# Performance work log

Hardware: AMD Instinct MI355X
Metric: run time of the kernel (lower is better)

Reference implementation:

```python
import jax, jax.numpy as jnp
import numpy as np

N = 1048576
B = 1024
H = 128
EPS = 1e-12  # F.normalize default eps


def setup_inputs() -> dict:
    key = jax.random.key(0)
    k1, k2, k3 = jax.random.split(key, 3)
    emb = jax.random.normal(k1, (N, H), dtype=jnp.float32)
    summary = jax.random.normal(k2, (B, H), dtype=jnp.float32)
    # CSR-style ptr: 0 = ptr[0] <= ... <= ptr[B] = N
    inner = jnp.sort(jax.random.randint(k3, (B - 1,), 0, N))
    ptr = jnp.concatenate([jnp.zeros((1,), jnp.int64),
                           inner.astype(jnp.int64),
                           jnp.full((1,), N, jnp.int64)])
    d = jnp.ones((H,), dtype=jnp.float32)
    scale = jnp.ones((1,), dtype=jnp.float32)
    return {"emb": emb, "summary": summary, "ptr": ptr, "d": d, "scale": scale}


def reference(emb, summary, ptr, d, scale):
    # L2-normalize each row (torch F.normalize: x / max(||x||, eps))
    norm = jnp.linalg.norm(emb, axis=-1, keepdims=True)
    emb_n = emb / jnp.maximum(norm, EPS)
    # node -> graph segment id from ptr (node i belongs to segment s iff ptr[s] <= i < ptr[s+1])
    seg = jnp.searchsorted(ptr[1:], jnp.arange(emb.shape[0]), side="right")  # [N]
    # fused diag-scale + per-graph ragged dot: out[n] = sum_h emb_n[n,h] * d[h] * summary[seg[n],h]
    s_per_node = summary[seg]  # [N, H] gather
    sim = jnp.sum(emb_n * d[None, :] * s_per_node, axis=-1)  # [N]
    return sim * scale[0]
```

## Files before the change

### kernel.cpp

```cpp
#include <hip/hip_runtime.h>
#include <math.h>


#define HDIM 128
#define NEPS 1e-12f

__global__ void seg_fill(const int* __restrict__ ptr, int* __restrict__ seg) {
    const int s  = blockIdx.x;
    const int lo = ptr[s], hi = ptr[s + 1];
    for (int i = lo + threadIdx.x; i < hi; i += blockDim.x)
        seg[i] = s;
}

__global__ void sd_fill(const float* __restrict__ summary,
                        const float* __restrict__ dvec,
                        const float* __restrict__ scale,
                        float* __restrict__ sd, int total) {
    const int i = blockIdx.x * blockDim.x + threadIdx.x;
    if (i < total) sd[i] = summary[i] * dvec[i & (HDIM - 1)] * scale[0];
}

__global__ __launch_bounds__(256) void sim_main(
    const float* __restrict__ emb,
    const float* __restrict__ sd,
    const int* __restrict__ seg,
    float* __restrict__ out, int N)
{
    const int tid = blockIdx.x * blockDim.x + threadIdx.x;
    const int sub = tid & 7;
    const long long row = (long long)(tid >> 3);
    if (row >= N) return;

    const int s = seg[row];
    const float4* e4 = (const float4*)(emb + row * (long long)HDIM);
    const float4* w4 = (const float4*)(sd + (long long)s * HDIM);

    float sumsq = 0.f, dot = 0.f;
    #pragma unroll
    for (int j = 0; j < 4; ++j) {
        const float4 e = e4[sub + 8 * j];
        const float4 w = w4[sub + 8 * j];
        sumsq = fmaf(e.x, e.x, sumsq); sumsq = fmaf(e.y, e.y, sumsq);
        sumsq = fmaf(e.z, e.z, sumsq); sumsq = fmaf(e.w, e.w, sumsq);
        dot   = fmaf(e.x, w.x, dot);   dot   = fmaf(e.y, w.y, dot);
        dot   = fmaf(e.z, w.z, dot);   dot   = fmaf(e.w, w.w, dot);
    }
    #pragma unroll
    for (int m = 4; m >= 1; m >>= 1) {
        sumsq += __shfl_xor(sumsq, m, 64);
        dot   += __shfl_xor(dot,   m, 64);
    }
    if (sub == 0)
        out[row] = dot / fmaxf(sqrtf(sumsq), NEPS);
}

__global__ __launch_bounds__(256) void sim_fallback(
    const float* __restrict__ emb, const float* __restrict__ summary,
    const int* __restrict__ ptr, const float* __restrict__ dvec,
    const float* __restrict__ scale, float* __restrict__ out, int N, int B)
{
    const int tid  = blockIdx.x * blockDim.x + threadIdx.x;
    const int lane = tid & 63;
    const int half = lane >> 5;
    const int l    = lane & 31;
    const long long row = (long long)(tid >> 6) * 2 + half;
    if (row >= N) return;
    int lo = 0, hi = B;
    while (lo < hi) {
        int mid = (lo + hi) >> 1;
        if (ptr[1 + mid] <= (int)row) lo = mid + 1; else hi = mid;
    }
    const float4* e4 = (const float4*)(emb + row * HDIM);
    const float4* s4 = (const float4*)(summary + (long long)lo * HDIM);
    const float4* d4 = (const float4*)dvec;
    const float4 e = e4[l], s = s4[l], dd = d4[l];
    float sumsq = e.x*e.x + e.y*e.y + e.z*e.z + e.w*e.w;
    float dot   = e.x*dd.x*s.x + e.y*dd.y*s.y + e.z*dd.z*s.z + e.w*dd.w*s.w;
    #pragma unroll
    for (int m = 16; m >= 1; m >>= 1) {
        sumsq += __shfl_xor(sumsq, m, 64);
        dot   += __shfl_xor(dot,   m, 64);
    }
    if (l == 0)
        out[row] = dot / fmaxf(sqrtf(sumsq), NEPS) * scale[0];
}

extern "C" void kernel_launch(void* const* d_in, const int* in_sizes, int n_in,
                              void* d_out, int out_size, void* d_ws, size_t ws_size,
                              hipStream_t stream) {
    const float* emb     = (const float*)d_in[0];
    const float* summary = (const float*)d_in[1];
    const int*   ptr     = (const int*)d_in[2];
    const float* dvec    = (const float*)d_in[3];
    const float* scale   = (const float*)d_in[4];
    float*       out     = (float*)d_out;

    const int Hn = in_sizes[3];
    const int N  = in_sizes[0] / Hn;
    const int B  = in_sizes[1] / Hn;

    const size_t sd_bytes  = (size_t)B * Hn * sizeof(float);
    const size_t seg_bytes = (size_t)N * sizeof(int);

    if (ws_size >= sd_bytes + seg_bytes) {
        float* sd  = (float*)d_ws;
        int*   seg = (int*)((char*)d_ws + sd_bytes);

        seg_fill<<<B, 256, 0, stream>>>(ptr, seg);
        const int sd_total = B * Hn;
        sd_fill<<<(sd_total + 255) / 256, 256, 0, stream>>>(summary, dvec,
                                                            scale, sd, sd_total);
        sim_main<<<(N + 31) / 32, 256, 0, stream>>>(emb, sd, seg, out, N);
    } else {
        sim_fallback<<<(N + 7) / 8, 256, 0, stream>>>(emb, summary, ptr, dvec,
                                                      scale, out, N, B);
    }
}
```

Before: 678.9 us.

## Fuse segment lookup and diag scaling into a single similarity kernel

Replaces the three-kernel pipeline (segment id fill, scaled summary precompute, main similarity) with one kernel. Each block binary-searches ptr for its first and last rows' segments into shared memory, then each row scans linearly between those bounds. The d vector and scale are applied inline, so the workspace writes and reads of seg and sd and two extra launches go away. The cost is a block-level barrier, extra ptr reads, and one extra dvec load per element.

```diff
diff --git a/kernel.cpp b/kernel.cpp
--- a/kernel.cpp
+++ b/kernel.cpp
@@ -4,46 +4,55 @@
 
 #define HDIM 128
 #define NEPS 1e-12f
+#define ROWS_PER_BLOCK 32
 
-__global__ void seg_fill(const int* __restrict__ ptr, int* __restrict__ seg) {
-    const int s  = blockIdx.x;
-    const int lo = ptr[s], hi = ptr[s + 1];
-    for (int i = lo + threadIdx.x; i < hi; i += blockDim.x)
-        seg[i] = s;
-}
+__global__ __launch_bounds__(256) void sim_fused(
+    const float* __restrict__ emb,
+    const float* __restrict__ summary,
+    const int*   __restrict__ ptr,
+    const float* __restrict__ dvec,
+    const float* __restrict__ scale,
+    float* __restrict__ out, int N, int B)
+{
+    __shared__ int s_bounds[2];
 
-__global__ void sd_fill(const float* __restrict__ summary,
-                        const float* __restrict__ dvec,
-                        const float* __restrict__ scale,
-                        float* __restrict__ sd, int total) {
-    const int i = blockIdx.x * blockDim.x + threadIdx.x;
-    if (i < total) sd[i] = summary[i] * dvec[i & (HDIM - 1)] * scale[0];
-}
+    const long long row0 = (long long)blockIdx.x * ROWS_PER_BLOCK;
 
-__global__ __launch_bounds__(256) void sim_main(
-    const float* __restrict__ emb,
-    const float* __restrict__ sd,
-    const int* __restrict__ seg,
-    float* __restrict__ out, int N)
-{
-    const int tid = blockIdx.x * blockDim.x + threadIdx.x;
-    const int sub = tid & 7;
-    const long long row = (long long)(tid >> 3);
+    if (threadIdx.x < 2) {
+        long long r = row0 + (threadIdx.x ? ROWS_PER_BLOCK - 1 : 0);
+        if (r > (long long)N - 1) r = (long long)N - 1;
+        int lo = 0, hi = B;
+        while (lo < hi) {
+            int mid = (lo + hi) >> 1;
+            if (ptr[1 + mid] <= (int)r) lo = mid + 1; else hi = mid;
+        }
+        s_bounds[threadIdx.x] = lo;
+    }
+    __syncthreads();
+    const int s0 = s_bounds[0];
+    const int s1 = s_bounds[1];
+
+    const int sub = threadIdx.x & 7;
+    const long long row = row0 + (threadIdx.x >> 3);
     if (row >= N) return;
 
-    const int s = seg[row];
+    int s = s0;
+    while (s < s1 && ptr[s + 1] <= (int)row) ++s;
+
     const float4* e4 = (const float4*)(emb + row * (long long)HDIM);
-    const float4* w4 = (const float4*)(sd + (long long)s * HDIM);
+    const float4* w4 = (const float4*)(summary + (long long)s * HDIM);
+    const float4* d4 = (const float4*)dvec;
 
     float sumsq = 0.f, dot = 0.f;
     #pragma unroll
     for (int j = 0; j < 4; ++j) {
-        const float4 e = e4[sub + 8 * j];
-        const float4 w = w4[sub + 8 * j];
+        const float4 e  = e4[sub + 8 * j];
+        const float4 w  = w4[sub + 8 * j];
+        const float4 dd = d4[sub + 8 * j];
         sumsq = fmaf(e.x, e.x, sumsq); sumsq = fmaf(e.y, e.y, sumsq);
         sumsq = fmaf(e.z, e.z, sumsq); sumsq = fmaf(e.w, e.w, sumsq);
-        dot   = fmaf(e.x, w.x, dot);   dot   = fmaf(e.y, w.y, dot);
-        dot   = fmaf(e.z, w.z, dot);   dot   = fmaf(e.w, w.w, dot);
+        dot = fmaf(e.x, w.x * dd.x, dot); dot = fmaf(e.y, w.y * dd.y, dot);
+        dot = fmaf(e.z, w.z * dd.z, dot); dot = fmaf(e.w, w.w * dd.w, dot);
     }
     #pragma unroll
     for (int m = 4; m >= 1; m >>= 1) {
@@ -51,37 +60,6 @@
         dot   += __shfl_xor(dot,   m, 64);
     }
     if (sub == 0)
-        out[row] = dot / fmaxf(sqrtf(sumsq), NEPS);
-}
-
-__global__ __launch_bounds__(256) void sim_fallback(
-    const float* __restrict__ emb, const float* __restrict__ summary,
-    const int* __restrict__ ptr, const float* __restrict__ dvec,
-    const float* __restrict__ scale, float* __restrict__ out, int N, int B)
-{
-    const int tid  = blockIdx.x * blockDim.x + threadIdx.x;
-    const int lane = tid & 63;
-    const int half = lane >> 5;
-    const int l    = lane & 31;
-    const long long row = (long long)(tid >> 6) * 2 + half;
-    if (row >= N) return;
-    int lo = 0, hi = B;
-    while (lo < hi) {
-        int mid = (lo + hi) >> 1;
-        if (ptr[1 + mid] <= (int)row) lo = mid + 1; else hi = mid;
-    }
-    const float4* e4 = (const float4*)(emb + row * HDIM);
-    const float4* s4 = (const float4*)(summary + (long long)lo * HDIM);
-    const float4* d4 = (const float4*)dvec;
-    const float4 e = e4[l], s = s4[l], dd = d4[l];
-    float sumsq = e.x*e.x + e.y*e.y + e.z*e.z + e.w*e.w;
-    float dot   = e.x*dd.x*s.x + e.y*dd.y*s.y + e.z*dd.z*s.z + e.w*dd.w*s.w;
-    #pragma unroll
-    for (int m = 16; m >= 1; m >>= 1) {
-        sumsq += __shfl_xor(sumsq, m, 64);
-        dot   += __shfl_xor(dot,   m, 64);
-    }
-    if (l == 0)
         out[row] = dot / fmaxf(sqrtf(sumsq), NEPS) * scale[0];
 }
 
@@ -99,20 +77,8 @@
     const int N  = in_sizes[0] / Hn;
     const int B  = in_sizes[1] / Hn;
 
-    const size_t sd_bytes  = (size_t)B * Hn * sizeof(float);
-    const size_t seg_bytes = (size_t)N * sizeof(int);
+    (void)d_ws; (void)ws_size; (void)n_in; (void)out_size;
 
-    if (ws_size >= sd_bytes + seg_bytes) {
-        float* sd  = (float*)d_ws;
-        int*   seg = (int*)((char*)d_ws + sd_bytes);
-
-        seg_fill<<<B, 256, 0, stream>>>(ptr, seg);
-        const int sd_total = B * Hn;
-        sd_fill<<<(sd_total + 255) / 256, 256, 0, stream>>>(summary, dvec,
-                                                            scale, sd, sd_total);
-        sim_main<<<(N + 31) / 32, 256, 0, stream>>>(emb, sd, seg, out, N);
-    } else {
-        sim_fallback<<<(N + 7) / 8, 256, 0, stream>>>(emb, summary, ptr, dvec,
-                                                      scale, out, N, B);
-    }
+    sim_fused<<<(N + ROWS_PER_BLOCK - 1) / ROWS_PER_BLOCK, 256, 0, stream>>>(
+        emb, summary, ptr, dvec, scale, out, N, B);
 }
```

Measured after the change: 689.7 us. Within noise of the previous version (+1.6%).
